# Optimization experiments

Measured on AMD Instinct MI355X. Metric: run time of the kernel, lower is better.

Reference implementation:

```python
import jax, jax.numpy as jnp
from jax import lax
import numpy as np


def _conv(x, w, b):
    y = lax.conv_general_dilated(x, w, (1, 1), 'VALID', dimension_numbers=('NCHW', 'OIHW', 'NCHW'))
    return y + b[None, :, None, None]


def _prelu(x, a):
    return jnp.where(x > 0, x, a[None, :, None, None] * x)


def _pnet(x, c1w, c1b, p1, c2w, c2b, p2, c3w, c3b, p3, w41, b41, w42, b42):
    x = _prelu(_conv(x, c1w, c1b), p1)
    H, W = x.shape[2], x.shape[3]
    # MaxPool2d(2,2, ceil_mode=True): pad bottom/right with -inf when odd
    x = lax.reduce_window(x, -jnp.inf, lax.max, (1, 1, 2, 2), (1, 1, 2, 2),
                          ((0, 0), (0, 0), (0, H % 2), (0, W % 2)))
    x = _prelu(_conv(x, c2w, c2b), p2)
    x = _prelu(_conv(x, c3w, c3b), p3)
    a = jax.nn.softmax(_conv(x, w41, b41), axis=1)
    b = _conv(x, w42, b42)
    return b, a


def _nms(boxes, scores, imgidx, valid, thr):
    # masked, fixed-size batched NMS (per-image via coordinate offset trick)
    N = boxes.shape[0]
    order = jnp.argsort(-jnp.where(valid, scores, -1e9))
    b = boxes[order] + imgidx[order].astype(boxes.dtype)[:, None] * 1e5
    v = valid[order]
    x1, y1, x2, y2 = b[:, 0], b[:, 1], b[:, 2], b[:, 3]
    area = jnp.maximum(x2 - x1, 0.0) * jnp.maximum(y2 - y1, 0.0)
    ar = jnp.arange(N)

    def body(i, keep):
        iw = jnp.maximum(jnp.minimum(x2[i], x2) - jnp.maximum(x1[i], x1), 0.0)
        ih = jnp.maximum(jnp.minimum(y2[i], y2) - jnp.maximum(y1[i], y1), 0.0)
        inter = iw * ih
        iou = inter / (area[i] + area - inter + 1e-9)
        return keep & ~((iou > thr) & (ar > i) & keep[i])

    keep = lax.fori_loop(0, N, body, v)
    return order, keep


def _detect(images, c1w, c1b, p1, c2w, c2b, p2, c3w, c3b, p3, w41, b41, w42, b42):
    params = (c1w, c1b, p1, c2w, c2b, p2, c3w, c3b, p3, w41, b41, w42, b42)
    x = jnp.transpose(images, (0, 3, 1, 2))  # NHWC -> NCHW
    B, _, H, W = x.shape
    m = 12.0 / 20.0  # 12 / minsize
    scales = []
    ml, si = min(H, W) * m, m
    while ml >= 12:
        scales.append(si)
        si *= 0.709
        ml *= 0.709
    KS, THR0 = 512, 0.6  # fixed per-scale candidate capacity
    all_b, all_i, all_k = [], [], []
    for scale in scales:
        nh, nw = int(H * scale + 1), int(W * scale + 1)
        im = jax.image.resize(x, (B, 3, nh, nw), method='linear')
        im = (im - 127.5) * 0.0078125
        reg, label = _pnet(im, *params)
        probs = label[:, 1]  # [B,h,w]
        b_, h_, w_ = probs.shape
        yy, xx = jnp.meshgrid(jnp.arange(h_), jnp.arange(w_), indexing='ij')
        bbx = jnp.tile(xx.reshape(-1), b_).astype(x.dtype)
        bby = jnp.tile(yy.reshape(-1), b_).astype(x.dtype)
        # stride=2, cellsize=12 grid-cell -> image-space boxes
        q = [jnp.floor((2 * bbx + 1) / scale), jnp.floor((2 * bby + 1) / scale),
             jnp.floor((2 * bbx + 12) / scale), jnp.floor((2 * bby + 12) / scale)]
        score = probs.reshape(-1)
        reg4 = jnp.transpose(reg, (0, 2, 3, 1)).reshape(-1, 4)
        boxes9 = jnp.concatenate([jnp.stack(q + [score], axis=1), reg4], axis=1)  # [N,9]
        imgidx = jnp.repeat(jnp.arange(b_), h_ * w_)
        k = min(KS, boxes9.shape[0])
        vals, idx = lax.top_k(jnp.where(score >= THR0, score, -1e9), k)
        bsel, isel, vsel = boxes9[idx], imgidx[idx], vals > -1e8
        order, keep = _nms(bsel[:, :4], bsel[:, 4], isel, vsel, 0.5)
        all_b.append(bsel[order])
        all_i.append(isel[order])
        all_k.append(keep)
    boxes = jnp.concatenate(all_b, 0)
    iidx = jnp.concatenate(all_i, 0)
    kp = jnp.concatenate(all_k, 0)
    K2 = min(1024, boxes.shape[0])
    vals, idx = lax.top_k(jnp.where(kp, boxes[:, 4], -1e9), K2)
    b2, i2, v2 = boxes[idx], iidx[idx], vals > -1e8
    order, keep = _nms(b2[:, :4], b2[:, 4], i2, v2, 0.7)
    b2 = b2[order]
    regw, regh = b2[:, 2] - b2[:, 0], b2[:, 3] - b2[:, 1]
    out = jnp.stack([b2[:, 0] + b2[:, 5] * regw, b2[:, 1] + b2[:, 6] * regh,
                     b2[:, 2] + b2[:, 7] * regw, b2[:, 3] + b2[:, 8] * regh, b2[:, 4]], axis=1)
    # rerec: square-ify
    hh, ww = out[:, 3] - out[:, 1], out[:, 2] - out[:, 0]
    l = jnp.maximum(hh, ww)
    x1 = out[:, 0] + ww * 0.5 - l * 0.5
    y1 = out[:, 1] + hh * 0.5 - l * 0.5
    out = jnp.stack([x1, y1, x1 + l, y1 + l, out[:, 4]], axis=1)
    return out * keep[:, None].astype(out.dtype)  # invalid/suppressed rows zeroed


def setup_inputs():
    key = jax.random.key(0)
    ks = jax.random.split(key, 16)
    rn = lambda k, s, sc=0.1: jax.random.normal(k, s, dtype=jnp.float32) * sc
    return {
        'images': jax.random.uniform(ks[0], (8, 768, 768, 3), dtype=jnp.float32) * 255.0,
        'c1w': rn(ks[1], (10, 3, 3, 3)), 'c1b': rn(ks[2], (10,)),
        'p1': 0.25 * jnp.ones((10,), jnp.float32),
        'c2w': rn(ks[3], (16, 10, 3, 3)), 'c2b': rn(ks[4], (16,)),
        'p2': 0.25 * jnp.ones((16,), jnp.float32),
        'c3w': rn(ks[5], (32, 16, 3, 3)), 'c3b': rn(ks[6], (32,)),
        'p3': 0.25 * jnp.ones((32,), jnp.float32),
        'w41': rn(ks[7], (2, 32, 1, 1)), 'b41': rn(ks[8], (2,)),
        'w42': rn(ks[9], (4, 32, 1, 1)), 'b42': rn(ks[10], (4,)),
    }


def reference(images, c1w, c1b, p1, c2w, c2b, p2, c3w, c3b, p3, w41, b41, w42, b42):
    return _detect(images, c1w, c1b, p1, c2w, c2b, p2, c3w, c3b, p3, w41, b41, w42, b42)
```

## Files before the change

kernel.cpp:

```cpp
#include <hip/hip_runtime.h>
#include <stdint.h>

typedef unsigned long long u64;
typedef unsigned int u32;

#define TPB 256
#define NJMAX 12
#define NSC 11

__device__ __forceinline__ int findJob(const int* cum, int nj, int v) {
  int j = 0;
  while (j + 1 < nj && v >= cum[j + 1]) ++j;
  return j;
}

struct MkP { int ns; int nw[NSC]; float invs[NSC], ks[NSC];
             int oxB[NSC], T[NSC], wOff[NSC]; };

__global__ void k_mkweights(int* __restrict__ tX0, int* __restrict__ tCNT,
                            float* __restrict__ tWT, float* __restrict__ tW, MkP P) {
  const int s = blockIdx.x;
  const int nw = P.nw[s];
  const float invs = P.invs[s], ks = P.ks[s];
  const int T = P.T[s];
  for (int ox = threadIdx.x; ox < nw; ox += TPB) {
    float sx = ((float)ox + 0.5f) * invs - 0.5f;
    int x0 = (int)ceilf(sx - ks); if (x0 < 0) x0 = 0;
    int x1 = (int)floorf(sx + ks); if (x1 > 767) x1 = 767;
    float wt = 0.f;
    float* wv = tW + P.wOff[s];
    for (int j = x0; j <= x1; ++j) {
      float w = fmaxf(0.f, 1.f - fabsf(sx - (float)j) / ks);
      wt += w;
      wv[(j - x0) * nw + ox] = w;
    }
    for (int k = x1 - x0 + 1; k < T; ++k) wv[k * nw + ox] = 0.f;
    int g = P.oxB[s] + ox;
    tX0[g] = x0; tCNT[g] = x1 - x0 + 1; tWT[g] = wt;
  }
}

struct DscP { int nj; int N[NJMAX]; int hOff[NJMAX], imgOff[NJMAX];
              int oxB[NJMAX], wOff[NJMAX];
              int cumW[NJMAX + 1], cumR[NJMAX + 1]; };

__global__ void k_mkdesc(int* __restrict__ hd, int* __restrict__ vd,
                         int hdcap, int vdcap, DscP P) {
  int gid = blockIdx.x * TPB + threadIdx.x;
  int totW = P.cumW[P.nj], totR = P.cumR[P.nj];
  if (gid < totW) {
    int j = findJob(P.cumW, P.nj, gid);
    int local = gid - P.cumW[j];
    int N = P.N[j];
    int ox = local % N, c = local / N;
    hd[gid]             = P.hOff[j] + c * 768 * N + ox;
    hd[hdcap + gid]     = c * 769;
    hd[2 * hdcap + gid] = N;
    hd[3 * hdcap + gid] = P.oxB[j] + ox;
    hd[4 * hdcap + gid] = P.wOff[j] + ox;
  }
  if (gid < totR) {
    int j = findJob(P.cumR, P.nj, gid);
    int local = gid - P.cumR[j];
    int N = P.N[j];
    int oy = local % N, q = local / N;
    vd[gid]             = P.hOff[j] + q * 768 * N;
    vd[vdcap + gid]     = P.imgOff[j] + (q * N + oy) * N;
    vd[2 * vdcap + gid] = P.oxB[j] + oy;
    vd[3 * vdcap + gid] = P.wOff[j] + oy;
    vd[4 * vdcap + gid] = N;
  }
}

__global__ void k_resizeH_d(const float* __restrict__ img, float* __restrict__ base,
                            const int* __restrict__ tX0, const int* __restrict__ tCNT,
                            const float* __restrict__ tWT, const float* __restrict__ tW,
                            const int* __restrict__ hd, int hdcap, int total) {
  __shared__ float row[3][769];
  const int y = blockIdx.x, b = blockIdx.y;
  const float* src = img + ((long)b * 768 + y) * 768 * 3;
  for (int t = threadIdx.x; t < 2304; t += TPB) {
    int x = t / 3, c = t - 3 * x;
    row[c][x] = src[t];
  }
  __syncthreads();
  const float* rowF = &row[0][0];
  const long yb = (long)y + 2304L * b;
  for (int t = threadIdx.x; t < total; t += TPB) {
    int A = hd[t];
    int R = hd[hdcap + t];
    int N = hd[2 * hdcap + t];
    int g = hd[3 * hdcap + t];
    int W = hd[4 * hdcap + t];
    int x0 = tX0[g], cnt = tCNT[g];
    float wt = tWT[g];
    const float* wv = tW + W;
    const float* rp = rowF + R + x0;
    float acc = 0.f;
    int k = 0;
    for (; k + 3 < cnt; k += 4) {
      float v0 = rp[k],     w0 = wv[(long)k * N];
      float v1 = rp[k + 1], w1 = wv[(long)(k + 1) * N];
      float v2 = rp[k + 2], w2 = wv[(long)(k + 2) * N];
      float v3 = rp[k + 3], w3 = wv[(long)(k + 3) * N];
      acc += v0 * w0; acc += v1 * w1; acc += v2 * w2; acc += v3 * w3;
    }
    for (; k < cnt; ++k) acc += rp[k] * wv[(long)k * N];
    base[(long)A + (long)N * yb] = acc / wt;
  }
}

__global__ void k_resizeV_row(const float* __restrict__ basep, float* __restrict__ img,
                              const int* __restrict__ tX0, const int* __restrict__ tCNT,
                              const float* __restrict__ tWT, const float* __restrict__ tW,
                              const int* __restrict__ vd, int vdcap, int nRows) {
  int row = blockIdx.x * 4 + (threadIdx.x >> 6);
  if (row >= nRows) return;
  int lane = threadIdx.x & 63;
  int S = vd[row];
  int O = vd[vdcap + row];
  int g = vd[2 * vdcap + row];
  int W = vd[3 * vdcap + row];
  int N = vd[4 * vdcap + row];
  int y0 = tX0[g], cnt = tCNT[g];
  float wt = tWT[g];
  const float* wv = tW + W;
  const float* col0 = basep + S + (long)y0 * N;
  for (int ox = lane; ox < N; ox += 64) {
    const float* col = col0 + ox;
    float acc = 0.f;
    int k = 0;
    for (; k + 3 < cnt; k += 4) {
      float v0 = col[(long)k * N],       w0 = wv[(long)k * N];
      float v1 = col[(long)(k + 1) * N], w1 = wv[(long)(k + 1) * N];
      float v2 = col[(long)(k + 2) * N], w2 = wv[(long)(k + 2) * N];
      float v3 = col[(long)(k + 3) * N], w3 = wv[(long)(k + 3) * N];
      acc += v0 * w0; acc += v1 * w1; acc += v2 * w2; acc += v3 * w3;
    }
    for (; k < cnt; ++k) acc += col[(long)k * N] * wv[(long)k * N];
    img[(long)O + ox] = (acc / wt - 127.5f) * 0.0078125f;
  }
}

__device__ __forceinline__ void conv1pool_body(
    const float* in, const float* w, const float* bias, const float* pr,
    float* out, int H, int W, int b, int px, int py) {
  const int h1 = H - 2, w1 = W - 2;
  const int PH = (h1 + 1) >> 1, PW = (w1 + 1) >> 1;
  if (px >= PW || py >= PH) return;
  const int x0 = px * 2, y0 = py * 2;
  float a00[10], a01[10], a10[10], a11[10];
#pragma unroll
  for (int co = 0; co < 10; ++co) { a00[co] = 0.f; a01[co] = 0.f; a10[co] = 0.f; a11[co] = 0.f; }
  const long HW = (long)H * W;
  const float* pp = in + ((long)b * 3 * H + y0) * W + x0;
  for (int ci = 0; ci < 3; ++ci, pp += HW) {
    const float* r = pp;
    float r00 = r[0], r01 = r[1], r02 = r[2], r03 = r[3]; r += W;
    float r10 = r[0], r11 = r[1], r12 = r[2], r13 = r[3]; r += W;
    float r20 = r[0], r21 = r[1], r22 = r[2], r23 = r[3]; r += W;
    float r30 = r[0], r31 = r[1], r32 = r[2], r33 = r[3];
#pragma unroll
    for (int co = 0; co < 10; ++co) {
      const float* wc = w + ((long)co * 3 + ci) * 9;
      float w0 = wc[0], w1_ = wc[1], w2 = wc[2];
      float w3 = wc[3], w4 = wc[4], w5 = wc[5];
      float w6 = wc[6], w7 = wc[7], w8 = wc[8];
      a00[co] += r00 * w0 + r01 * w1_ + r02 * w2;
      a00[co] += r10 * w3 + r11 * w4 + r12 * w5;
      a00[co] += r20 * w6 + r21 * w7 + r22 * w8;
      a01[co] += r01 * w0 + r02 * w1_ + r03 * w2;
      a01[co] += r11 * w3 + r12 * w4 + r13 * w5;
      a01[co] += r21 * w6 + r22 * w7 + r23 * w8;
      a10[co] += r10 * w0 + r11 * w1_ + r12 * w2;
      a10[co] += r20 * w3 + r21 * w4 + r22 * w5;
      a10[co] += r30 * w6 + r31 * w7 + r32 * w8;
      a11[co] += r11 * w0 + r12 * w1_ + r13 * w2;
      a11[co] += r21 * w3 + r22 * w4 + r23 * w5;
      a11[co] += r31 * w6 + r32 * w7 + r33 * w8;
    }
  }
  const bool vx = (x0 + 1 < w1), vy = (y0 + 1 < h1);
#pragma unroll
  for (int co = 0; co < 10; ++co) {
    const float bb = bias[co], al = pr[co];
    float v = a00[co] + bb; v = v > 0.f ? v : al * v;
    float m = v;
    if (vx) { v = a01[co] + bb; v = v > 0.f ? v : al * v; m = fmaxf(m, v); }
    if (vy) { v = a10[co] + bb; v = v > 0.f ? v : al * v; m = fmaxf(m, v); }
    if (vx && vy) { v = a11[co] + bb; v = v > 0.f ? v : al * v; m = fmaxf(m, v); }
    out[(((long)b * 10 + co) * PH + py) * PW + px] = m;
  }
}

struct C1P { int nj; int nh[NJMAX]; int imgOff[NJMAX], poolOff[NJMAX];
             int t1x[NJMAX]; int cumT[NJMAX + 1]; };

__global__ void k_conv1pool_job(const float* __restrict__ imgb, const float* __restrict__ w,
                                const float* __restrict__ bias, const float* __restrict__ pr,
                                float* __restrict__ poolb, C1P P) {
  int j = findJob(P.cumT, P.nj, blockIdx.x);
  int local = blockIdx.x - P.cumT[j];
  int t1x = P.t1x[j];
  int tX = local % t1x, tY = local / t1x;
  conv1pool_body(imgb + P.imgOff[j], w, bias, pr, poolb + P.poolOff[j],
                 P.nh[j], P.nh[j], blockIdx.z,
                 tX * 16 + (threadIdx.x & 15), tY * 16 + (threadIdx.x >> 4));
}

__device__ __forceinline__ void conv3x3c8_body(
    const float* in, const float* w, const float* bias, const float* pr,
    float* out, int Cin, int Cout, int H, int W, int cog, int b, int x0, int y) {
  const int OH = H - 2, OW = W - 2;
  if (y >= OH || x0 >= OW) return;
  float acc[8][4];
#pragma unroll
  for (int k = 0; k < 8; ++k) { acc[k][0] = 0.f; acc[k][1] = 0.f; acc[k][2] = 0.f; acc[k][3] = 0.f; }
  const float* wp = w + (long)cog * Cin * 9;
  const long HW = (long)H * W;
  const float* pp = in + ((long)b * Cin * H + y) * W + x0;
  for (int ci = 0; ci < Cin; ++ci, pp += HW) {
    const float* r = pp;
    float q00 = r[0], q01 = r[1], q02 = r[2], q03 = r[3], q04 = r[4], q05 = r[5]; r += W;
    float q10 = r[0], q11 = r[1], q12 = r[2], q13 = r[3], q14 = r[4], q15 = r[5]; r += W;
    float q20 = r[0], q21 = r[1], q22 = r[2], q23 = r[3], q24 = r[4], q25 = r[5];
#pragma unroll
    for (int k = 0; k < 8; ++k) {
      const float* wc = wp + ((long)k * Cin + ci) * 9;
      float w0 = wc[0], w1 = wc[1], w2 = wc[2];
      float w3 = wc[3], w4 = wc[4], w5 = wc[5];
      float w6 = wc[6], w7 = wc[7], w8 = wc[8];
      acc[k][0] += q00 * w0 + q01 * w1 + q02 * w2;
      acc[k][1] += q01 * w0 + q02 * w1 + q03 * w2;
      acc[k][2] += q02 * w0 + q03 * w1 + q04 * w2;
      acc[k][3] += q03 * w0 + q04 * w1 + q05 * w2;
      acc[k][0] += q10 * w3 + q11 * w4 + q12 * w5;
      acc[k][1] += q11 * w3 + q12 * w4 + q13 * w5;
      acc[k][2] += q12 * w3 + q13 * w4 + q14 * w5;
      acc[k][3] += q13 * w3 + q14 * w4 + q15 * w5;
      acc[k][0] += q20 * w6 + q21 * w7 + q22 * w8;
      acc[k][1] += q21 * w6 + q22 * w7 + q23 * w8;
      acc[k][2] += q22 * w6 + q23 * w7 + q24 * w8;
      acc[k][3] += q23 * w6 + q24 * w7 + q25 * w8;
    }
  }
  const int rem = OW - x0;
#pragma unroll
  for (int k = 0; k < 8; ++k) {
    const int co = cog + k;
    const float bb = bias[co], al = pr[co];
    float* op = out + (((long)b * Cout + co) * OH + y) * OW + x0;
    float v0 = acc[k][0] + bb; v0 = v0 > 0.f ? v0 : al * v0;
    op[0] = v0;
    if (rem > 1) { float v = acc[k][1] + bb; v = v > 0.f ? v : al * v; op[1] = v; }
    if (rem > 2) { float v = acc[k][2] + bb; v = v > 0.f ? v : al * v; op[2] = v; }
    if (rem > 3) { float v = acc[k][3] + bb; v = v > 0.f ? v : al * v; op[3] = v; }
  }
}

struct CvP { int nj; int H[NJMAX]; int inOff[NJMAX], outOff[NJMAX];
             int tx[NJMAX]; int cumT[NJMAX + 1]; };

__global__ void k_conv3x3c8_job(const float* __restrict__ inb, const float* __restrict__ w,
                                const float* __restrict__ bias, const float* __restrict__ pr,
                                float* __restrict__ outb, int Cin, int Cout, CvP P) {
  int j = findJob(P.cumT, P.nj, blockIdx.x);
  int local = blockIdx.x - P.cumT[j];
  int tx0 = P.tx[j];
  int tX = local % tx0, tY = local / tx0;
  conv3x3c8_body(inb + P.inOff[j], w, bias, pr, outb + P.outOff[j], Cin, Cout,
                 P.H[j], P.H[j], blockIdx.y * 8, blockIdx.z,
                 tX * 64 + (threadIdx.x & 15) * 4, tY * 16 + (threadIdx.x >> 4));
}

__device__ __forceinline__ void head_body(const float* x3, const float* w41,
                                          const float* b41, const float* w42,
                                          const float* b42, float* reg, u64* keys,
                                          int plane, long idx) {
  int b = (int)(idx / plane); int rem = (int)(idx % plane);
  const float* p = x3 + (long)b * 32 * plane + rem;
  float l0 = 0.f, l1 = 0.f, r0 = 0.f, r1 = 0.f, r2 = 0.f, r3 = 0.f;
  for (int c = 0; c < 32; ++c) {
    float v = p[(long)c * plane];
    l0 += v * w41[c];      l1 += v * w41[32 + c];
    r0 += v * w42[c];      r1 += v * w42[32 + c];
    r2 += v * w42[64 + c]; r3 += v * w42[96 + c];
  }
  l0 += b41[0]; l1 += b41[1];
  r0 += b42[0]; r1 += b42[1]; r2 += b42[2]; r3 += b42[3];
  float mx = fmaxf(l0, l1);
  float e0 = expf(l0 - mx), e1 = expf(l1 - mx);
  float s = e1 / (e0 + e1);
  reg[idx * 4 + 0] = r0; reg[idx * 4 + 1] = r1;
  reg[idx * 4 + 2] = r2; reg[idx * 4 + 3] = r3;
  u32 ic = 0xFFFFFFFFu - (u32)idx;
  u64 k = (s >= 0.6f) ? ((((u64)__float_as_uint(s)) << 32) | ic) : (u64)ic;
  keys[idx] = k;
}

struct HdP { int nj; int h3[NJMAX]; int c3Off[NJMAX], kOff[NJMAX];
             int cumC[NJMAX + 1]; };

__global__ void k_head_job(const float* __restrict__ c3b, const float* __restrict__ w41,
                           const float* __restrict__ b41, const float* __restrict__ w42,
                           const float* __restrict__ b42, float* __restrict__ regb,
                           u64* __restrict__ keysb, HdP P) {
  int gid = blockIdx.x * TPB + threadIdx.x;
  if (gid >= P.cumC[P.nj]) return;
  int j = findJob(P.cumC, P.nj, gid);
  int idx = gid - P.cumC[j];
  head_body(c3b + P.c3Off[j], w41, b41, w42, b42,
            regb + 4L * P.kOff[j], keysb + P.kOff[j], P.h3[j] * P.h3[j], idx);
}

__device__ __forceinline__ void bitonic2048(u64* s) {
  for (int k = 2; k <= 2048; k <<= 1) {
    for (int j = k >> 1; j > 0; j >>= 1) {
      for (int i = threadIdx.x; i < 2048; i += TPB) {
        int ixj = i ^ j;
        if (ixj > i) {
          u64 a = s[i], b = s[ixj];
          bool desc = ((i & k) == 0);
          if (desc ? (a < b) : (a > b)) { s[i] = b; s[ixj] = a; }
        }
      }
      __syncthreads();
    }
  }
}

__global__ void k_topk(const u64* __restrict__ in, int n, u64* __restrict__ out, int K) {
  __shared__ u64 s[2048];
  int base = blockIdx.x * 2048;
  for (int t = threadIdx.x; t < 2048; t += TPB) {
    int gi = base + t;
    s[t] = (gi < n) ? in[gi] : 0ULL;
  }
  __syncthreads();
  bitonic2048(s);
  for (int t = threadIdx.x; t < K; t += TPB)
    out[(long)blockIdx.x * K + t] = s[t];
}

struct TkP { int nj; int srcSel[NJMAX]; int srcOff[NJMAX]; int n[NJMAX];
             int dstOff[NJMAX]; int cumB[NJMAX + 1]; };

__global__ void k_topk_job(u64* __restrict__ A, u64* __restrict__ B, TkP P) {
  __shared__ u64 s[2048];
  int j = findJob(P.cumB, P.nj, blockIdx.x);
  int lb = blockIdx.x - P.cumB[j];
  const u64* src = (P.srcSel[j] ? B : A) + P.srcOff[j];
  u64* dst = (P.srcSel[j] ? A : B) + P.dstOff[j];
  int n = P.n[j];
  int base = lb * 2048;
  for (int t = threadIdx.x; t < 2048; t += TPB) {
    int gi = base + t;
    s[t] = (gi < n) ? src[gi] : 0ULL;
  }
  __syncthreads();
  bitonic2048(s);
  for (int t = threadIdx.x; t < 512; t += TPB)
    dst[(long)lb * 512 + t] = s[t];
}

struct TkFP { int nj; int srcSel[NJMAX]; int srcOff[NJMAX]; int n[NJMAX]; int sIdx[NJMAX]; };

__global__ void k_topk_fin(const u64* __restrict__ A, const u64* __restrict__ B,
                           u64* __restrict__ selk, TkFP P) {
  __shared__ u64 s[2048];
  int j = blockIdx.x;
  const u64* src = (P.srcSel[j] ? B : A) + P.srcOff[j];
  int n = P.n[j];
  for (int t = threadIdx.x; t < 2048; t += TPB)
    s[t] = (t < n) ? src[t] : 0ULL;
  __syncthreads();
  bitonic2048(s);
  for (int t = threadIdx.x; t < 512; t += TPB)
    selk[(long)P.sIdx[j] * 512 + t] = s[t];
}

__device__ __forceinline__ void gather_body(const u64* keys, const float* reg,
                                            float* boxes, int h, int w, float scalef,
                                            int i) {
  float* bx = boxes + (long)i * 12;
  u64 key = keys[i];
  if ((key >> 32) == 0ULL) {
    for (int q = 0; q < 12; ++q) bx[q] = 0.f;
    return;
  }
  u32 cell = 0xFFFFFFFFu - (u32)(key & 0xFFFFFFFFu);
  int x = (int)(cell % (u32)w); u32 t2 = cell / (u32)w;
  int y = (int)(t2 % (u32)h); int b = (int)(t2 / (u32)h);
  float fx = (float)x, fy = (float)y;
  bx[0] = floorf((2.f * fx + 1.f) / scalef);
  bx[1] = floorf((2.f * fy + 1.f) / scalef);
  bx[2] = floorf((2.f * fx + 12.f) / scalef);
  bx[3] = floorf((2.f * fy + 12.f) / scalef);
  bx[4] = __uint_as_float((u32)(key >> 32));
  bx[5] = reg[(long)cell * 4 + 0];
  bx[6] = reg[(long)cell * 4 + 1];
  bx[7] = reg[(long)cell * 4 + 2];
  bx[8] = reg[(long)cell * 4 + 3];
  bx[9] = (float)b;
  bx[10] = 1.f;
  bx[11] = 0.f;
}

struct GtP { int nj; int h3[NJMAX]; float scalef[NJMAX]; int kOff[NJMAX]; int sIdx[NJMAX]; };

__global__ void k_gather_job(const u64* __restrict__ selk, const float* __restrict__ regb,
                             float* __restrict__ boxes, GtP P) {
  int j = blockIdx.x >> 1;
  int i = ((blockIdx.x & 1) << 8) + threadIdx.x;
  gather_body(selk + (long)P.sIdx[j] * 512, regb + 4L * P.kOff[j],
              boxes + (long)P.sIdx[j] * 512 * 12, P.h3[j], P.h3[j], P.scalef[j], i);
}

__global__ void k_nms(float* __restrict__ boxes, int per, float thr) {
  __shared__ float sx1[1024], sy1[1024], sx2[1024], sy2[1024], sar[1024];
  __shared__ unsigned char kp[1024];
  __shared__ unsigned char kb[64];
  __shared__ int snv;
  float* bs = boxes + (long)blockIdx.x * per * 12;
  int N = per;
  if (threadIdx.x == 0) snv = 0;
  __syncthreads();
  for (int i = threadIdx.x; i < N; i += blockDim.x) {
    const float* b = bs + (long)i * 12;
    float off = b[9] * 100000.0f;
    float a0 = b[0] + off, a1 = b[1] + off, a2 = b[2] + off, a3 = b[3] + off;
    sx1[i] = a0; sy1[i] = a1; sx2[i] = a2; sy2[i] = a3;
    sar[i] = fmaxf(a2 - a0, 0.f) * fmaxf(a3 - a1, 0.f);
    bool v = (b[10] != 0.f);
    kp[i] = v;
    if (v) atomicMax(&snv, i + 1);
  }
  __syncthreads();
  int nv = snv;
  const int wave = threadIdx.x >> 6, lane = threadIdx.x & 63;
  for (int base = 0; base < nv; base += 64) {
    const int lim = (nv - base < 64) ? (nv - base) : 64;
    if (wave == 0) {
      int gi = base + lane;
      bool ok = (lane < lim) && kp[gi];
      float bx1 = 0.f, by1 = 0.f, bx2 = 0.f, by2 = 0.f, ba = 0.f;
      if (lane < lim) { bx1 = sx1[gi]; by1 = sy1[gi]; bx2 = sx2[gi]; by2 = sy2[gi]; ba = sar[gi]; }
      for (int i = 0; i < lim; ++i) {
        int ki = __shfl((int)ok, i);
        float xi1 = __shfl(bx1, i), yi1 = __shfl(by1, i);
        float xi2 = __shfl(bx2, i), yi2 = __shfl(by2, i);
        float ai = __shfl(ba, i);
        if (ki && lane > i && ok) {
          float iw = fmaxf(fminf(xi2, bx2) - fmaxf(xi1, bx1), 0.f);
          float ih = fmaxf(fminf(yi2, by2) - fmaxf(yi1, by1), 0.f);
          float inter = iw * ih;
          float iou = inter / (ai + ba - inter + 1e-9f);
          if (iou > thr) ok = false;
        }
      }
      if (lane < lim) kp[gi] = ok ? 1 : 0;
      kb[lane] = (lane < lim && ok) ? 1 : 0;
    }
    __syncthreads();
    for (int j = base + 64 + threadIdx.x; j < nv; j += blockDim.x) {
      if (!kp[j]) continue;
      float jx2 = sx2[j], jy2 = sy2[j], jx1 = sx1[j], jy1 = sy1[j], ja = sar[j];
      bool ok = true;
      for (int i = 0; i < lim && ok; ++i) {
        if (!kb[i]) continue;
        int gi = base + i;
        float iw = fmaxf(fminf(sx2[gi], jx2) - fmaxf(sx1[gi], jx1), 0.f);
        float ih = fmaxf(fminf(sy2[gi], jy2) - fmaxf(sy1[gi], jy1), 0.f);
        float inter = iw * ih;
        float iou = inter / (sar[gi] + ja - inter + 1e-9f);
        if (iou > thr) ok = false;
      }
      if (!ok) kp[j] = 0;
    }
    __syncthreads();
  }
  for (int i = threadIdx.x; i < N; i += blockDim.x)
    bs[(long)i * 12 + 11] = kp[i] ? 1.f : 0.f;
}

__global__ void k_finalkeys(const float* __restrict__ boxes, u64* __restrict__ keys,
                            int total, int padded) {
  int i = blockIdx.x * blockDim.x + threadIdx.x;
  if (i >= padded) return;
  u64 k = 0ULL;
  if (i < total) {
    const float* b = boxes + (long)i * 12;
    u32 ic = 0xFFFFFFFFu - (u32)i;
    k = (b[11] != 0.f) ? ((((u64)__float_as_uint(b[4])) << 32) | ic) : (u64)ic;
  }
  keys[i] = k;
}

__global__ void k_gatherfinal(const u64* __restrict__ keys, const float* __restrict__ boxes,
                              float* __restrict__ sel) {
  int i = blockIdx.x * blockDim.x + threadIdx.x;
  if (i >= 1024) return;
  u64 key = keys[i];
  float* o = sel + (long)i * 12;
  if ((key >> 32) == 0ULL) {
    for (int q = 0; q < 12; ++q) o[q] = 0.f;
    return;
  }
  u32 bi = 0xFFFFFFFFu - (u32)(key & 0xFFFFFFFFu);
  const float* b = boxes + (long)bi * 12;
  for (int q = 0; q < 12; ++q) o[q] = b[q];
  o[10] = 1.f;
  o[11] = 0.f;
}

__global__ void k_refine(const float* __restrict__ sel, float* __restrict__ out, int N) {
  int i = blockIdx.x * blockDim.x + threadIdx.x;
  if (i >= N) return;
  const float* b = sel + (long)i * 12;
  float keep = b[11];
  float x1 = b[0], y1 = b[1], x2 = b[2], y2 = b[3], sc = b[4];
  float rw = x2 - x1, rh = y2 - y1;
  float o0 = x1 + b[5] * rw;
  float o1 = y1 + b[6] * rh;
  float o2 = x2 + b[7] * rw;
  float o3 = y2 + b[8] * rh;
  float hh = o3 - o1, ww = o2 - o0;
  float l = fmaxf(hh, ww);
  float nx1 = o0 + ww * 0.5f - l * 0.5f;
  float ny1 = o1 + hh * 0.5f - l * 0.5f;
  out[(long)i * 5 + 0] = nx1 * keep;
  out[(long)i * 5 + 1] = ny1 * keep;
  out[(long)i * 5 + 2] = (nx1 + l) * keep;
  out[(long)i * 5 + 3] = (ny1 + l) * keep;
  out[(long)i * 5 + 4] = sc * keep;
}

extern "C" void kernel_launch(void* const* d_in, const int* in_sizes, int n_in,
                              void* d_out, int out_size, void* d_ws, size_t ws_size,
                              hipStream_t stream) {
  (void)in_sizes; (void)n_in; (void)out_size;
  const float* images = (const float*)d_in[0];
  const float* c1w = (const float*)d_in[1];
  const float* c1b = (const float*)d_in[2];
  const float* p1  = (const float*)d_in[3];
  const float* c2w = (const float*)d_in[4];
  const float* c2b = (const float*)d_in[5];
  const float* p2  = (const float*)d_in[6];
  const float* c3w = (const float*)d_in[7];
  const float* c3b = (const float*)d_in[8];
  const float* p3  = (const float*)d_in[9];
  const float* w41 = (const float*)d_in[10];
  const float* b41 = (const float*)d_in[11];
  const float* w42 = (const float*)d_in[12];
  const float* b42 = (const float*)d_in[13];
  float* ws = (float*)d_ws;

  double scl[16]; int nsc = 0;
  {
    double m = 12.0 / 20.0;
    double ml = 768.0 * m;
    double si = m;
    while (ml >= 12.0) { scl[nsc++] = si; si *= 0.709; ml *= 0.709; }
  }

  auto cdiv = [](long a, long b) { return (int)((a + b - 1) / b); };

  int NH[NSC], PH_[NSC], H2[NSC], H3[NSC], OXB[NSC], TT[NSC], WOFF[NSC];
  float INV[NSC], KSF[NSC];
  {
    int oxb = 0, woff = 0;
    for (int s = 0; s < nsc; ++s) {
      int nh = (int)(768.0 * scl[s] + 1.0);
      NH[s] = nh;
      PH_[s] = ((nh - 2) + 1) / 2;
      H2[s] = PH_[s] - 2;
      H3[s] = H2[s] - 2;
      double inv = 1.0 / (((double)nh) / 768.0);
      INV[s] = (float)inv;
      KSF[s] = (float)(inv > 1.0 ? inv : 1.0);
      TT[s] = (int)(2.0f * KSF[s]) + 2;
      OXB[s] = oxb; oxb += nh;
      WOFF[s] = woff; woff += nh * TT[s];
    }
  }

  static const int GA[11] = {0, 1, 2, 3, 4, 5, 6, 7, 8, 9, 10};
  static const int G1[7] = {0, 5, 6, 7, 8, 9, 10};
  static const int G2[4] = {1, 2, 3, 4};

  struct Layout {
    long HT, IMG, POOL, C2, REG, KEYS, SCR, SEL, BOX, FK, FS, SF, TBL, HD, VD, extent;
    int hdcap, vdcap;
  };

  auto calcLayout = [&](const int* const* gps, const int* gn, int ng,
                        int hdcap, int vdcap, Layout& L) {
    long htA = 0, c3A = 0, imgA = 0, poolA = 0, c2A = 0, cellsA = 0, scrA = 0;
    for (int g = 0; g < ng; ++g) {
      long ht = 0, c3 = 0, im = 0, pl = 0, c2s = 0, ck = 0, sc = 0;
      for (int q = 0; q < gn[g]; ++q) {
        int s = gps[g][q];
        ht += 24L * 768 * NH[s];
        im += 24L * NH[s] * NH[s];
        pl += 80L * PH_[s] * PH_[s];
        c2s += 128L * H2[s] * H2[s];
        c3 += 256L * H3[s] * H3[s];
        long cells = 8L * H3[s] * H3[s];
        ck += cells;
        sc += 512L * ((cells + 2047) / 2048);
      }
      if (ht > htA) htA = ht; if (c3 > c3A) c3A = c3; if (im > imgA) imgA = im;
      if (pl > poolA) poolA = pl; if (c2s > c2A) c2A = c2s;
      if (ck > cellsA) cellsA = ck; if (sc > scrA) scrA = sc;
    }
    long htR = htA > c3A ? htA : c3A;
    auto al = [](long v) { return (v + 15) & ~15L; };
    long off = 0;
    L.HT = off;   off += al(htR);
    L.IMG = off;  off += al(imgA);
    L.POOL = off; off += al(poolA);
    L.C2 = off;   off += al(c2A);
    L.REG = off;  off += al(4 * cellsA);
    L.KEYS = off; off += al(2 * cellsA);
    L.SCR = off;  off += al(2 * scrA + 16384);
    L.SEL = off;  off += al(11264);
    L.BOX = off;  off += al(67584);
    L.FK = off;   off += al(16384);
    L.FS = off;   off += al(2048);
    L.SF = off;   off += al(12288);
    L.TBL = off;  off += al(12288 + 24000);
    L.HD = off;   off += al((long)ng * 5 * hdcap);
    L.VD = off;   off += al((long)ng * 5 * vdcap);
    L.extent = off;
    L.hdcap = hdcap; L.vdcap = vdcap;
  };

  Layout LA, LB;
  {
    const int* gpsA[1] = {GA}; int gnA[1] = {11};
    calcLayout(gpsA, gnA, 1, 8192, 56320, LA);
    const int* gpsB[2] = {G1, G2}; int gnB[2] = {7, 4};
    calcLayout(gpsB, gnB, 2, 2560, 20480, LB);
  }
  bool big = (ws_size >= (size_t)LA.extent * 4);
  const Layout& L = big ? LA : LB;
  const int* GS[2]; int GN[2]; int ngroups;
  if (big) { GS[0] = GA; GN[0] = 11; ngroups = 1; }
  else { GS[0] = G1; GN[0] = 7; GS[1] = G2; GN[1] = 4; ngroups = 2; }

  u64* keys  = (u64*)(ws + L.KEYS);
  u64* scr   = (u64*)(ws + L.SCR);
  u64* selk  = (u64*)(ws + L.SEL);
  u64* fkeys = (u64*)(ws + L.FK);
  u64* fsel  = (u64*)(ws + L.FS);
  float* boxes = ws + L.BOX;
  float* self  = ws + L.SF;
  int*   tX0  = (int*)(ws + L.TBL);
  int*   tCNT = (int*)(ws + L.TBL + 4096);
  float* tWT  = ws + L.TBL + 8192;
  float* tW   = ws + L.TBL + 12288;

  {
    MkP P; P.ns = nsc;
    for (int s = 0; s < nsc; ++s) {
      P.nw[s] = NH[s]; P.invs[s] = INV[s]; P.ks[s] = KSF[s];
      P.oxB[s] = OXB[s]; P.T[s] = TT[s]; P.wOff[s] = WOFF[s];
    }
    k_mkweights<<<nsc, TPB, 0, stream>>>(tX0, tCNT, tWT, tW, P);
  }

  int imgOff[2][NJMAX], poolOff[2][NJMAX], c2Off[2][NJMAX], c3Off[2][NJMAX],
      htOff[2][NJMAX], kOff[2][NJMAX], cells[2][NJMAX];
  int cumWtot[2], cumRtot[2];
  for (int g = 0; g < ngroups; ++g) {
    long ch = 0, ci = 0, cp = 0, c2 = 0, c3 = 0, ck = 0;
    int cw = 0, cr = 0;
    for (int q = 0; q < GN[g]; ++q) {
      int s = GS[g][q];
      htOff[g][q] = (int)ch;  ch += 24L * 768 * NH[s];
      imgOff[g][q] = (int)ci; ci += 24L * NH[s] * NH[s];
      poolOff[g][q] = (int)cp; cp += 80L * PH_[s] * PH_[s];
      c2Off[g][q] = (int)c2;  c2 += 128L * H2[s] * H2[s];
      c3Off[g][q] = (int)c3;  c3 += 256L * H3[s] * H3[s];
      kOff[g][q] = (int)ck;   cells[g][q] = 8 * H3[s] * H3[s]; ck += cells[g][q];
      cw += 3 * NH[s]; cr += 24 * NH[s];
    }
    cumWtot[g] = cw; cumRtot[g] = cr;
  }

  for (int g = 0; g < ngroups; ++g) {
    DscP P; P.nj = GN[g];
    int cw = 0, cr = 0;
    for (int q = 0; q < GN[g]; ++q) {
      int s = GS[g][q];
      P.N[q] = NH[s]; P.hOff[q] = htOff[g][q]; P.imgOff[q] = imgOff[g][q];
      P.oxB[q] = OXB[s]; P.wOff[q] = WOFF[s];
      P.cumW[q] = cw; cw += 3 * NH[s];
      P.cumR[q] = cr; cr += 24 * NH[s];
    }
    P.cumW[GN[g]] = cw; P.cumR[GN[g]] = cr;
    int* hd = (int*)(ws + L.HD) + (long)g * 5 * L.hdcap;
    int* vd = (int*)(ws + L.VD) + (long)g * 5 * L.vdcap;
    int tot = cw > cr ? cw : cr;
    k_mkdesc<<<cdiv(tot, TPB), TPB, 0, stream>>>(hd, vd, L.hdcap, L.vdcap, P);
  }

  for (int g = 0; g < ngroups; ++g) {
    const int* gs = GS[g];
    int nj = GN[g];
    int* hd = (int*)(ws + L.HD) + (long)g * 5 * L.hdcap;
    int* vd = (int*)(ws + L.VD) + (long)g * 5 * L.vdcap;
    {
      dim3 gh(768, 8, 1);
      k_resizeH_d<<<gh, TPB, 0, stream>>>(images, ws + L.HT, tX0, tCNT, tWT, tW,
                                          hd, L.hdcap, cumWtot[g]);
    }
    k_resizeV_row<<<cdiv(cumRtot[g], 4), TPB, 0, stream>>>(
        ws + L.HT, ws + L.IMG, tX0, tCNT, tWT, tW, vd, L.vdcap, cumRtot[g]);
    {
      C1P P; P.nj = nj; int ct = 0;
      for (int q = 0; q < nj; ++q) {
        int s = gs[q];
        P.nh[q] = NH[s];
        P.imgOff[q] = imgOff[g][q]; P.poolOff[q] = poolOff[g][q];
        int t1x = cdiv(PH_[s], 16);
        P.t1x[q] = t1x;
        P.cumT[q] = ct; ct += t1x * t1x;
      }
      P.cumT[nj] = ct;
      dim3 gg(ct, 1, 8);
      k_conv1pool_job<<<gg, TPB, 0, stream>>>(ws + L.IMG, c1w, c1b, p1, ws + L.POOL, P);
    }
    {
      CvP P; P.nj = nj; int ct = 0;
      for (int q = 0; q < nj; ++q) {
        int s = gs[q];
        P.H[q] = PH_[s];
        P.inOff[q] = poolOff[g][q]; P.outOff[q] = c2Off[g][q];
        int tx = cdiv(H2[s], 64), ty = cdiv(H2[s], 16);
        P.tx[q] = tx;
        P.cumT[q] = ct; ct += tx * ty;
      }
      P.cumT[nj] = ct;
      dim3 gg(ct, 2, 8);
      k_conv3x3c8_job<<<gg, TPB, 0, stream>>>(ws + L.POOL, c2w, c2b, p2, ws + L.C2,
                                              10, 16, P);
    }
    {
      CvP P; P.nj = nj; int ct = 0;
      for (int q = 0; q < nj; ++q) {
        int s = gs[q];
        P.H[q] = H2[s];
        P.inOff[q] = c2Off[g][q]; P.outOff[q] = c3Off[g][q];
        int tx = cdiv(H3[s], 64), ty = cdiv(H3[s], 16);
        P.tx[q] = tx;
        P.cumT[q] = ct; ct += tx * ty;
      }
      P.cumT[nj] = ct;
      dim3 gg(ct, 4, 8);
      k_conv3x3c8_job<<<gg, TPB, 0, stream>>>(ws + L.C2, c3w, c3b, p3, ws + L.HT,
                                              16, 32, P);
    }
    {
      HdP P; P.nj = nj; int cc = 0;
      for (int q = 0; q < nj; ++q) {
        int s = gs[q];
        P.h3[q] = H3[s];
        P.c3Off[q] = c3Off[g][q]; P.kOff[q] = kOff[g][q];
        P.cumC[q] = cc; cc += cells[g][q];
      }
      P.cumC[nj] = cc;
      k_head_job<<<cdiv(cc, TPB), TPB, 0, stream>>>(ws + L.HT, w41, b41, w42, b42,
                                                    ws + L.REG, keys, P);
    }
    {
      int bOff[NJMAX];
      {
        int c = 0;
        for (int q = 0; q < nj; ++q) { bOff[q] = c; c += 512 * cdiv(cells[g][q], 2048); }
      }
      long nCur[NJMAX]; int par[NJMAX];
      for (int q = 0; q < nj; ++q) { nCur[q] = cells[g][q]; par[q] = 0; }
      while (true) {
        TkP P; P.nj = 0; int cum = 0; int act[NJMAX];
        for (int q = 0; q < nj; ++q) {
          if (nCur[q] > 2048) {
            int r = P.nj++;
            act[r] = q;
            int blocks = cdiv(nCur[q], 2048);
            P.srcSel[r] = par[q];
            P.srcOff[r] = par[q] ? bOff[q] : kOff[g][q];
            P.dstOff[r] = par[q] ? kOff[g][q] : bOff[q];
            P.n[r] = (int)nCur[q];
            P.cumB[r] = cum; cum += blocks;
          }
        }
        P.cumB[P.nj] = cum;
        if (P.nj == 0) break;
        k_topk_job<<<cum, TPB, 0, stream>>>(keys, scr, P);
        for (int r = 0; r < P.nj; ++r) {
          int q = act[r];
          nCur[q] = 512L * cdiv(nCur[q], 2048);
          par[q] ^= 1;
        }
      }
      TkFP F; F.nj = nj;
      for (int q = 0; q < nj; ++q) {
        F.srcSel[q] = par[q];
        F.srcOff[q] = par[q] ? bOff[q] : kOff[g][q];
        F.n[q] = (int)nCur[q];
        F.sIdx[q] = gs[q];
      }
      k_topk_fin<<<nj, TPB, 0, stream>>>(keys, scr, selk, F);
    }
    {
      GtP P; P.nj = nj;
      for (int q = 0; q < nj; ++q) {
        int s = gs[q];
        P.h3[q] = H3[s]; P.scalef[q] = (float)scl[s]; P.kOff[q] = kOff[g][q];
        P.sIdx[q] = s;
      }
      k_gather_job<<<2 * nj, TPB, 0, stream>>>(selk, ws + L.REG, boxes, P);
    }
  }

  k_nms<<<nsc, TPB, 0, stream>>>(boxes, 512, 0.5f);

  int total = nsc * 512;
  k_finalkeys<<<cdiv(8192, TPB), TPB, 0, stream>>>(boxes, fkeys, total, 8192);
  k_topk<<<4, TPB, 0, stream>>>(fkeys, 8192, scr, 1024);
  k_topk<<<2, TPB, 0, stream>>>(scr, 4096, keys, 1024);
  k_topk<<<1, TPB, 0, stream>>>(keys, 2048, fsel, 1024);
  k_gatherfinal<<<4, TPB, 0, stream>>>(fsel, boxes, self);
  k_nms<<<1, TPB, 0, stream>>>(self, 1024, 0.7f);
  k_refine<<<4, TPB, 0, stream>>>(self, (float*)d_out, 1024);
}
```

Baseline: 1.114 ms.

## Fuse final key build, top-k sort, gather, NMS and refine into one kernel

Replaces the tail of seven small launches (key build, three bitonic top-k passes, gather, single-block NMS, refine) with one 1024-thread block kernel. That kernel sorts all 8192 keys in shared memory with a single bitonic sort, gathers the top 1024, runs a wave-level shuffle-based NMS and writes the refined boxes. Separately, the resize kernels switch their index arithmetic from 64-bit to 32-bit. The fused tail removes launch overhead and global round trips, but it runs on a single block and does a full 8192-element sort instead of a tree of smaller sorts.

```diff
diff --git a/kernel.cpp b/kernel.cpp
--- a/kernel.cpp
+++ b/kernel.cpp
@@ -99,13 +99,13 @@
     float acc = 0.f;
     int k = 0;
     for (; k + 3 < cnt; k += 4) {
-      float v0 = rp[k],     w0 = wv[(long)k * N];
-      float v1 = rp[k + 1], w1 = wv[(long)(k + 1) * N];
-      float v2 = rp[k + 2], w2 = wv[(long)(k + 2) * N];
-      float v3 = rp[k + 3], w3 = wv[(long)(k + 3) * N];
+      float v0 = rp[k],     w0 = wv[k * N];
+      float v1 = rp[k + 1], w1 = wv[(k + 1) * N];
+      float v2 = rp[k + 2], w2 = wv[(k + 2) * N];
+      float v3 = rp[k + 3], w3 = wv[(k + 3) * N];
       acc += v0 * w0; acc += v1 * w1; acc += v2 * w2; acc += v3 * w3;
     }
-    for (; k < cnt; ++k) acc += rp[k] * wv[(long)k * N];
+    for (; k < cnt; ++k) acc += rp[k] * wv[k * N];
     base[(long)A + (long)N * yb] = acc / wt;
   }
 }
@@ -131,13 +131,13 @@
     float acc = 0.f;
     int k = 0;
     for (; k + 3 < cnt; k += 4) {
-      float v0 = col[(long)k * N],       w0 = wv[(long)k * N];
-      float v1 = col[(long)(k + 1) * N], w1 = wv[(long)(k + 1) * N];
-      float v2 = col[(long)(k + 2) * N], w2 = wv[(long)(k + 2) * N];
-      float v3 = col[(long)(k + 3) * N], w3 = wv[(long)(k + 3) * N];
+      float v0 = col[k * N],       w0 = wv[k * N];
+      float v1 = col[(k + 1) * N], w1 = wv[(k + 1) * N];
+      float v2 = col[(k + 2) * N], w2 = wv[(k + 2) * N];
+      float v3 = col[(k + 3) * N], w3 = wv[(k + 3) * N];
       acc += v0 * w0; acc += v1 * w1; acc += v2 * w2; acc += v3 * w3;
     }
-    for (; k < cnt; ++k) acc += col[(long)k * N] * wv[(long)k * N];
+    for (; k < cnt; ++k) acc += col[k * N] * wv[k * N];
     img[(long)O + ox] = (acc / wt - 127.5f) * 0.0078125f;
   }
 }
@@ -329,19 +329,6 @@
   }
 }
 
-__global__ void k_topk(const u64* __restrict__ in, int n, u64* __restrict__ out, int K) {
-  __shared__ u64 s[2048];
-  int base = blockIdx.x * 2048;
-  for (int t = threadIdx.x; t < 2048; t += TPB) {
-    int gi = base + t;
-    s[t] = (gi < n) ? in[gi] : 0ULL;
-  }
-  __syncthreads();
-  bitonic2048(s);
-  for (int t = threadIdx.x; t < K; t += TPB)
-    out[(long)blockIdx.x * K + t] = s[t];
-}
-
 struct TkP { int nj; int srcSel[NJMAX]; int srcOff[NJMAX]; int n[NJMAX];
              int dstOff[NJMAX]; int cumB[NJMAX + 1]; };
 
@@ -483,56 +470,132 @@
     bs[(long)i * 12 + 11] = kp[i] ? 1.f : 0.f;
 }
 
-__global__ void k_finalkeys(const float* __restrict__ boxes, u64* __restrict__ keys,
-                            int total, int padded) {
-  int i = blockIdx.x * blockDim.x + threadIdx.x;
-  if (i >= padded) return;
-  u64 k = 0ULL;
-  if (i < total) {
-    const float* b = boxes + (long)i * 12;
-    u32 ic = 0xFFFFFFFFu - (u32)i;
-    k = (b[11] != 0.f) ? ((((u64)__float_as_uint(b[4])) << 32) | ic) : (u64)ic;
-  }
-  keys[i] = k;
-}
-
-__global__ void k_gatherfinal(const u64* __restrict__ keys, const float* __restrict__ boxes,
-                              float* __restrict__ sel) {
-  int i = blockIdx.x * blockDim.x + threadIdx.x;
-  if (i >= 1024) return;
-  u64 key = keys[i];
-  float* o = sel + (long)i * 12;
-  if ((key >> 32) == 0ULL) {
-    for (int q = 0; q < 12; ++q) o[q] = 0.f;
-    return;
-  }
-  u32 bi = 0xFFFFFFFFu - (u32)(key & 0xFFFFFFFFu);
-  const float* b = boxes + (long)bi * 12;
-  for (int q = 0; q < 12; ++q) o[q] = b[q];
-  o[10] = 1.f;
-  o[11] = 0.f;
-}
-
-__global__ void k_refine(const float* __restrict__ sel, float* __restrict__ out, int N) {
-  int i = blockIdx.x * blockDim.x + threadIdx.x;
-  if (i >= N) return;
-  const float* b = sel + (long)i * 12;
-  float keep = b[11];
-  float x1 = b[0], y1 = b[1], x2 = b[2], y2 = b[3], sc = b[4];
-  float rw = x2 - x1, rh = y2 - y1;
-  float o0 = x1 + b[5] * rw;
-  float o1 = y1 + b[6] * rh;
-  float o2 = x2 + b[7] * rw;
-  float o3 = y2 + b[8] * rh;
-  float hh = o3 - o1, ww = o2 - o0;
-  float l = fmaxf(hh, ww);
-  float nx1 = o0 + ww * 0.5f - l * 0.5f;
-  float ny1 = o1 + hh * 0.5f - l * 0.5f;
-  out[(long)i * 5 + 0] = nx1 * keep;
-  out[(long)i * 5 + 1] = ny1 * keep;
-  out[(long)i * 5 + 2] = (nx1 + l) * keep;
-  out[(long)i * 5 + 3] = (ny1 + l) * keep;
-  out[(long)i * 5 + 4] = sc * keep;
+__global__ void k_final(const float* __restrict__ boxes, int total, float thr,
+                        float* __restrict__ selfb, float* __restrict__ out) {
+  __shared__ u64 s[8192];
+  __shared__ unsigned char kb[64];
+  __shared__ int snv;
+  float* fb = (float*)s;
+  const int tid = threadIdx.x;
+  for (int i = tid; i < 8192; i += 1024) {
+    u64 k = 0ULL;
+    if (i < total) {
+      const float* b = boxes + (long)i * 12;
+      u32 ic = 0xFFFFFFFFu - (u32)i;
+      k = (b[11] != 0.f) ? ((((u64)__float_as_uint(b[4])) << 32) | ic) : (u64)ic;
+    }
+    s[i] = k;
+  }
+  if (tid == 0) snv = 0;
+  __syncthreads();
+  for (int k = 2; k <= 8192; k <<= 1) {
+    for (int j = k >> 1; j > 0; j >>= 1) {
+      for (int i = tid; i < 8192; i += 1024) {
+        int ixj = i ^ j;
+        if (ixj > i) {
+          u64 a = s[i], b = s[ixj];
+          bool desc = ((i & k) == 0);
+          if (desc ? (a < b) : (a > b)) { s[i] = b; s[ixj] = a; }
+        }
+      }
+      __syncthreads();
+    }
+  }
+  u64 myKey = s[tid];
+  __syncthreads();
+  float* sx1 = fb;
+  float* sy1 = fb + 1024;
+  float* sx2 = fb + 2048;
+  float* sy2 = fb + 3072;
+  float* sar = fb + 4096;
+  unsigned char* kp = (unsigned char*)(fb + 5120);
+  {
+    int i = tid;
+    float* o = selfb + (long)i * 12;
+    if ((myKey >> 32) == 0ULL) {
+      for (int q = 0; q < 12; ++q) o[q] = 0.f;
+      sx1[i] = 0.f; sy1[i] = 0.f; sx2[i] = 0.f; sy2[i] = 0.f; sar[i] = 0.f;
+      kp[i] = 0;
+    } else {
+      u32 bi = 0xFFFFFFFFu - (u32)(myKey & 0xFFFFFFFFu);
+      const float* b = boxes + (long)bi * 12;
+      float r0 = b[0], r1 = b[1], r2 = b[2], r3 = b[3], r4 = b[4];
+      float r5 = b[5], r6 = b[6], r7 = b[7], r8 = b[8], r9 = b[9];
+      o[0] = r0; o[1] = r1; o[2] = r2; o[3] = r3; o[4] = r4;
+      o[5] = r5; o[6] = r6; o[7] = r7; o[8] = r8; o[9] = r9;
+      o[10] = 1.f; o[11] = 0.f;
+      float off = r9 * 100000.0f;
+      float a0 = r0 + off, a1 = r1 + off, a2 = r2 + off, a3 = r3 + off;
+      sx1[i] = a0; sy1[i] = a1; sx2[i] = a2; sy2[i] = a3;
+      sar[i] = fmaxf(a2 - a0, 0.f) * fmaxf(a3 - a1, 0.f);
+      kp[i] = 1;
+      atomicMax(&snv, i + 1);
+    }
+  }
+  __syncthreads();
+  int nv = snv;
+  const int wave = tid >> 6, lane = tid & 63;
+  for (int base = 0; base < nv; base += 64) {
+    const int lim = (nv - base < 64) ? (nv - base) : 64;
+    if (wave == 0) {
+      int gi = base + lane;
+      bool ok = (lane < lim) && kp[gi];
+      float bx1 = 0.f, by1 = 0.f, bx2 = 0.f, by2 = 0.f, ba = 0.f;
+      if (lane < lim) { bx1 = sx1[gi]; by1 = sy1[gi]; bx2 = sx2[gi]; by2 = sy2[gi]; ba = sar[gi]; }
+      for (int i = 0; i < lim; ++i) {
+        int ki = __shfl((int)ok, i);
+        float xi1 = __shfl(bx1, i), yi1 = __shfl(by1, i);
+        float xi2 = __shfl(bx2, i), yi2 = __shfl(by2, i);
+        float ai = __shfl(ba, i);
+        if (ki && lane > i && ok) {
+          float iw = fmaxf(fminf(xi2, bx2) - fmaxf(xi1, bx1), 0.f);
+          float ih = fmaxf(fminf(yi2, by2) - fmaxf(yi1, by1), 0.f);
+          float inter = iw * ih;
+          float iou = inter / (ai + ba - inter + 1e-9f);
+          if (iou > thr) ok = false;
+        }
+      }
+      if (lane < lim) kp[gi] = ok ? 1 : 0;
+      kb[lane] = (lane < lim && ok) ? 1 : 0;
+    }
+    __syncthreads();
+    for (int j = base + 64 + tid; j < nv; j += blockDim.x) {
+      if (!kp[j]) continue;
+      float jx2 = sx2[j], jy2 = sy2[j], jx1 = sx1[j], jy1 = sy1[j], ja = sar[j];
+      bool ok = true;
+      for (int i = 0; i < lim && ok; ++i) {
+        if (!kb[i]) continue;
+        int gi = base + i;
+        float iw = fmaxf(fminf(sx2[gi], jx2) - fmaxf(sx1[gi], jx1), 0.f);
+        float ih = fmaxf(fminf(sy2[gi], jy2) - fmaxf(sy1[gi], jy1), 0.f);
+        float inter = iw * ih;
+        float iou = inter / (sar[gi] + ja - inter + 1e-9f);
+        if (iou > thr) ok = false;
+      }
+      if (!ok) kp[j] = 0;
+    }
+    __syncthreads();
+  }
+  {
+    int i = tid;
+    const float* b = selfb + (long)i * 12;
+    float keep = kp[i] ? 1.f : 0.f;
+    float x1 = b[0], y1 = b[1], x2 = b[2], y2 = b[3], sc = b[4];
+    float rw = x2 - x1, rh = y2 - y1;
+    float o0 = x1 + b[5] * rw;
+    float o1 = y1 + b[6] * rh;
+    float o2 = x2 + b[7] * rw;
+    float o3 = y2 + b[8] * rh;
+    float hh = o3 - o1, ww = o2 - o0;
+    float l = fmaxf(hh, ww);
+    float nx1 = o0 + ww * 0.5f - l * 0.5f;
+    float ny1 = o1 + hh * 0.5f - l * 0.5f;
+    out[(long)i * 5 + 0] = nx1 * keep;
+    out[(long)i * 5 + 1] = ny1 * keep;
+    out[(long)i * 5 + 2] = (nx1 + l) * keep;
+    out[(long)i * 5 + 3] = (ny1 + l) * keep;
+    out[(long)i * 5 + 4] = sc * keep;
+  }
 }
 
 extern "C" void kernel_launch(void* const* d_in, const int* in_sizes, int n_in,
@@ -651,8 +714,6 @@
   u64* keys  = (u64*)(ws + L.KEYS);
   u64* scr   = (u64*)(ws + L.SCR);
   u64* selk  = (u64*)(ws + L.SEL);
-  u64* fkeys = (u64*)(ws + L.FK);
-  u64* fsel  = (u64*)(ws + L.FS);
   float* boxes = ws + L.BOX;
   float* self  = ws + L.SF;
   int*   tX0  = (int*)(ws + L.TBL);
@@ -827,11 +888,5 @@
   k_nms<<<nsc, TPB, 0, stream>>>(boxes, 512, 0.5f);
 
   int total = nsc * 512;
-  k_finalkeys<<<cdiv(8192, TPB), TPB, 0, stream>>>(boxes, fkeys, total, 8192);
-  k_topk<<<4, TPB, 0, stream>>>(fkeys, 8192, scr, 1024);
-  k_topk<<<2, TPB, 0, stream>>>(scr, 4096, keys, 1024);
-  k_topk<<<1, TPB, 0, stream>>>(keys, 2048, fsel, 1024);
-  k_gatherfinal<<<4, TPB, 0, stream>>>(fsel, boxes, self);
-  k_nms<<<1, TPB, 0, stream>>>(self, 1024, 0.7f);
-  k_refine<<<4, TPB, 0, stream>>>(self, (float*)d_out, 1024);
-}
+  k_final<<<1, 1024, 0, stream>>>(boxes, total, 0.7f, self, (float*)d_out);
+}
```

Result: faster. 1.016 ms (-8.8%).
